# Kernel optimization log

Measured on AMD Instinct MI355X. Metric: run time of the kernel, lower is better.

The kernel has to match this reference:

```python
import jax, jax.numpy as jnp
import numpy as np

N_NODES = 100000
N_EDGES = 1600000
IN_CH = 128
HID = 128
OUT_CH = 10


def setup_inputs() -> dict:
    key = jax.random.key(0)
    ks = jax.random.split(key, 14)
    s_in = 1.0 / np.sqrt(IN_CH)
    s_h = 1.0 / np.sqrt(HID)
    return {
        "x0": jax.random.normal(ks[0], (N_NODES, IN_CH), jnp.float32),
        "edge_index": jax.random.randint(ks[1], (2, N_EDGES), 0, N_NODES, jnp.int32),
        "edge_weight": jax.random.uniform(ks[2], (N_EDGES,), jnp.float32),
        # GraphConv layer 1 (in -> hid): lin_rel (weight+bias) applied to aggregated msgs, lin_root (no bias)
        "W1_rel": jax.random.uniform(ks[3], (IN_CH, HID), jnp.float32, -s_in, s_in),
        "b1": jax.random.uniform(ks[4], (HID,), jnp.float32, -s_in, s_in),
        "W1_root": jax.random.uniform(ks[5], (IN_CH, HID), jnp.float32, -s_in, s_in),
        # GraphConv layer 2 (hid -> hid)
        "W2_rel": jax.random.uniform(ks[6], (HID, HID), jnp.float32, -s_h, s_h),
        "b2": jax.random.uniform(ks[7], (HID,), jnp.float32, -s_h, s_h),
        "W2_root": jax.random.uniform(ks[8], (HID, HID), jnp.float32, -s_h, s_h),
        # GraphConv layer 3 (hid -> hid)
        "W3_rel": jax.random.uniform(ks[9], (HID, HID), jnp.float32, -s_h, s_h),
        "b3": jax.random.uniform(ks[10], (HID,), jnp.float32, -s_h, s_h),
        "W3_root": jax.random.uniform(ks[11], (HID, HID), jnp.float32, -s_h, s_h),
        # classification head
        "W_lin": jax.random.uniform(ks[12], (HID, OUT_CH), jnp.float32, -s_h, s_h),
        "b_lin": jax.random.uniform(ks[13], (OUT_CH,), jnp.float32, -s_h, s_h),
    }


def _graph_conv(x, src, dst, ew, W_rel, b_rel, W_root):
    # message: x_j * w_e ; aggregate: scatter-add onto dst ; update: lin_rel(agg) + lin_root(x)
    msg = x[src] * ew[:, None]                                   # [E, C]
    agg = jax.ops.segment_sum(msg, dst, num_segments=x.shape[0])  # [N, C]
    return agg @ W_rel + b_rel + x @ W_root                      # [N, C']


def reference(x0, edge_index, edge_weight,
              W1_rel, b1, W1_root,
              W2_rel, b2, W2_root,
              W3_rel, b3, W3_root,
              W_lin, b_lin):
    src, dst = edge_index[0], edge_index[1]
    # dropout p=0.2 is identity in eval mode
    x1 = jax.nn.relu(_graph_conv(x0, src, dst, edge_weight, W1_rel, b1, W1_root))
    x2 = jax.nn.relu(_graph_conv(x1, src, dst, edge_weight, W2_rel, b2, W2_root))
    x3 = jax.nn.relu(_graph_conv(x2, src, dst, edge_weight, W3_rel, b3, W3_root))
    logits = x3 @ W_lin + b_lin
    return jax.nn.log_softmax(logits, axis=-1)
```

## Files before the change

### kernel.cpp

```cpp
#include <hip/hip_runtime.h>
#include <hip/hip_bf16.h>
#include <math.h>

#define C128 128
#define OUT_CH 10

typedef __attribute__((ext_vector_type(8))) short short8;
typedef __attribute__((ext_vector_type(4))) float f32x4;
typedef __attribute__((ext_vector_type(2))) float f32x2;
typedef __attribute__((ext_vector_type(4))) int i32x4;

__device__ __forceinline__ unsigned short f2bf(float f) {
    unsigned b = __float_as_uint(f);
    unsigned r = (b + 0x7FFF + ((b >> 16) & 1)) >> 16;
    return (unsigned short)r;
}
__device__ __forceinline__ float bf2f(unsigned short u) {
    return __uint_as_float(((unsigned)u) << 16);
}


#define NBMAX 400
#define BCAP  4608
#define P1K   4096

__global__ __launch_bounds__(512) void bin_kernel(
    const int* __restrict__ ei, const float* __restrict__ ew,
    int* __restrict__ gcur, uint2* __restrict__ bins, int E, int nb)
{
    __shared__ int cnt[NBMAX];
    __shared__ int pos[NBMAX];
    __shared__ int gbase[NBMAX];
    __shared__ int s[512];
    __shared__ int totalSh;
    __shared__ uint2 buf[P1K];

    const int t = threadIdx.x;
    const int e0 = blockIdx.x * P1K;

    for (int b = t; b < nb; b += 512) { cnt[b] = 0; pos[b] = 0; }
    __syncthreads();

    unsigned rec[8];
    int dstv[8];
    const int e = e0 + t * 8;
    if (e + 8 <= E) {
        i32x4 d0 = __builtin_nontemporal_load((const i32x4*)(ei + E + e));
        i32x4 d1 = __builtin_nontemporal_load((const i32x4*)(ei + E + e + 4));
        i32x4 s0 = __builtin_nontemporal_load((const i32x4*)(ei + e));
        i32x4 s1 = __builtin_nontemporal_load((const i32x4*)(ei + e + 4));
        f32x4 w0 = __builtin_nontemporal_load((const f32x4*)(ew + e));
        f32x4 w1 = __builtin_nontemporal_load((const f32x4*)(ew + e + 4));
        int dd[8] = {d0.x, d0.y, d0.z, d0.w, d1.x, d1.y, d1.z, d1.w};
        int ss[8] = {s0.x, s0.y, s0.z, s0.w, s1.x, s1.y, s1.z, s1.w};
        float ww[8] = {w0.x, w0.y, w0.z, w0.w, w1.x, w1.y, w1.z, w1.w};
#pragma unroll
        for (int j = 0; j < 8; ++j) {
            unsigned wb = __float_as_uint(ww[j]);
            unsigned r  = ((wb + 0x7FFF + ((wb >> 16) & 1)) >> 16) & 0x7FFFu;
            rec[j]  = (unsigned)ss[j] | (r << 17);
            dstv[j] = dd[j];
            atomicAdd(&cnt[dd[j] >> 8], 1);
        }
    } else {
#pragma unroll
        for (int j = 0; j < 8; ++j) {
            int ee = e + j;
            if (ee < E) {
                int dst = ei[E + ee];
                unsigned wb = __float_as_uint(ew[ee]);
                unsigned r  = ((wb + 0x7FFF + ((wb >> 16) & 1)) >> 16) & 0x7FFFu;
                rec[j]  = (unsigned)ei[ee] | (r << 17);
                dstv[j] = dst;
                atomicAdd(&cnt[dst >> 8], 1);
            } else {
                dstv[j] = -1;
            }
        }
    }
    __syncthreads();

    int c = (t < nb) ? cnt[t] : 0;
    s[t] = c;
    __syncthreads();
    for (int o = 1; o < 512; o <<= 1) {
        int u = (t >= o) ? s[t - o] : 0;
        __syncthreads();
        s[t] += u;
        __syncthreads();
    }
    if (t == nb - 1) totalSh = s[t];
    __syncthreads();

#pragma unroll
    for (int j = 0; j < 8; ++j) {
        if (dstv[j] >= 0) {
            int b = dstv[j] >> 8;
            int r = atomicAdd(&pos[b], 1);
            buf[s[b] - cnt[b] + r] = make_uint2(rec[j], (unsigned)dstv[j]);
        }
    }
    __syncthreads();

    if (t < nb) {
        int b = t + (int)((blockIdx.x * 131u) % (unsigned)nb);
        if (b >= nb) b -= nb;
        int cb = cnt[b];
        if (cb > 0) gbase[b] = atomicAdd(&gcur[b], cb);
    }
    __syncthreads();

    const int total = totalSh;
    for (int i = t; i < total; i += 512) {
        uint2 v = buf[i];
        int b = (int)(v.y >> 8);
        int dest = gbase[b] + (i - (s[b] - cnt[b]));
        if (dest < BCAP) bins[(size_t)b * BCAP + dest] = v;
    }
}

__global__ __launch_bounds__(512) void bucket_scan_kernel(
    const int* __restrict__ gcur, int* __restrict__ bbase,
    int* __restrict__ row_ptr, int nb, int N, int E)
{
    __shared__ int s[512];
    int t = threadIdx.x;
    int v = (t < nb) ? gcur[t] : 0;
    s[t] = v;
    __syncthreads();
    for (int o = 1; o < 512; o <<= 1) {
        int u = (t >= o) ? s[t - o] : 0;
        __syncthreads();
        s[t] += u;
        __syncthreads();
    }
    if (t < nb) bbase[t] = s[t] - v;
    if (t == 0) row_ptr[N] = E;
}

__global__ __launch_bounds__(256) void build_kernel(
    const uint2* __restrict__ bins, const int* __restrict__ gcur,
    const int* __restrict__ bbase, int* __restrict__ row_ptr,
    unsigned* __restrict__ csr, int N)
{
    __shared__ int rowCnt[256];
    __shared__ int rowOff[256];
    __shared__ int sc[256];
    __shared__ unsigned out[BCAP];

    const int b = blockIdx.x, t = threadIdx.x;
    int cnt = gcur[b];
    if (cnt > BCAP) cnt = BCAP;
    const int base = bbase[b];
    const uint2* mb = bins + (size_t)b * BCAP;

    rowCnt[t] = 0;
    __syncthreads();
    for (int i = t; i < cnt; i += 256) atomicAdd(&rowCnt[(int)(mb[i].y & 255u)], 1);
    __syncthreads();

    int v = rowCnt[t];
    sc[t] = v;
    __syncthreads();
    for (int o = 1; o < 256; o <<= 1) {
        int u = (t >= o) ? sc[t - o] : 0;
        __syncthreads();
        sc[t] += u;
        __syncthreads();
    }
    rowOff[t] = sc[t] - v;
    int idx = b * 256 + t;
    if (idx <= N) row_ptr[idx] = base + sc[t] - v;
    rowCnt[t] = 0;
    __syncthreads();

    for (int i = t; i < cnt; i += 256) {
        uint2 r = mb[i];
        int d = (int)(r.y & 255u);
        int k = atomicAdd(&rowCnt[d], 1);
        out[rowOff[d] + k] = r.x;
    }
    __syncthreads();

    for (int i = t; i < cnt; i += 256) csr[base + i] = out[i];
}


__global__ __launch_bounds__(256) void cvt_both_kernel(const float4* __restrict__ x,
                                                       ushort4* __restrict__ xb,
                                                       unsigned* __restrict__ xf8, int n4) {
    int i = blockIdx.x * blockDim.x + threadIdx.x;
    if (i < n4) {
        float4 v = x[i];
        ushort4 o;
        o.x = f2bf(v.x); o.y = f2bf(v.y); o.z = f2bf(v.z); o.w = f2bf(v.w);
        xb[i] = o;
        unsigned p = __builtin_amdgcn_cvt_pk_fp8_f32(v.x, v.y, 0, false);
        p = __builtin_amdgcn_cvt_pk_fp8_f32(v.z, v.w, p, true);
        xf8[i] = p;
    }
}


__global__ __launch_bounds__(256) void pack_w_kernel(const float* __restrict__ Wr,
                                                     const float* __restrict__ Wt,
                                                     unsigned short* __restrict__ Wp) {
    int idx = blockIdx.x * 256 + threadIdx.x;
    int j    = idx & 7;
    int n    = (idx >> 3) & 127;
    int quad = (idx >> 10) & 3;
    int ks   = idx >> 12;
    const float* W = (ks < 4) ? Wr : Wt;
    int k = (ks & 3) * 32 + quad * 8 + j;
    Wp[idx] = f2bf(W[(size_t)k * C128 + n]);
}


__global__ __launch_bounds__(256) void gather_fp8_kernel(
    const unsigned* __restrict__ xf8,
    const int* __restrict__ row_ptr,
    const unsigned* __restrict__ csr, unsigned short* __restrict__ aggb, int N)
{
    int node = blockIdx.x * 4 + (threadIdx.x >> 6);
    if (node >= N) return;
    int lane = threadIdx.x & 63;
    int g   = lane >> 4;
    int l16 = lane & 15;
    int i0  = row_ptr[node];
    int deg = row_ptr[node + 1] - i0;

    f32x2 acc2[4];
#pragma unroll
    for (int j = 0; j < 4; ++j) acc2[j] = (f32x2){0.f, 0.f};

    for (int base = 0; base < deg; base += 64) {
        int rem = deg - base; if (rem > 64) rem = 64;
        int rec = 0;
        if (base + lane < deg) rec = (int)csr[i0 + base + lane];

        int c = 0;
        for (; c + 16 <= rem; c += 16) {
            int s0 = __shfl(rec, c + g,      64);
            int s1 = __shfl(rec, c + 4 + g,  64);
            int s2 = __shfl(rec, c + 8 + g,  64);
            int s3 = __shfl(rec, c + 12 + g, 64);
            float w0 = __uint_as_float(((unsigned)s0 >> 17) << 16);
            float w1 = __uint_as_float(((unsigned)s1 >> 17) << 16);
            float w2 = __uint_as_float(((unsigned)s2 >> 17) << 16);
            float w3 = __uint_as_float(((unsigned)s3 >> 17) << 16);
            uint2 q0 = *(const uint2*)&xf8[(size_t)(s0 & 0x1FFFF) * 32 + l16 * 2];
            uint2 q1 = *(const uint2*)&xf8[(size_t)(s1 & 0x1FFFF) * 32 + l16 * 2];
            uint2 q2 = *(const uint2*)&xf8[(size_t)(s2 & 0x1FFFF) * 32 + l16 * 2];
            uint2 q3 = *(const uint2*)&xf8[(size_t)(s3 & 0x1FFFF) * 32 + l16 * 2];
#define ACCUM(q, wv)                                                         \
            {                                                                \
                f32x2 w2v = {(wv), (wv)};                                    \
                acc2[0] += __builtin_amdgcn_cvt_pk_f32_fp8((q).x, false) * w2v; \
                acc2[1] += __builtin_amdgcn_cvt_pk_f32_fp8((q).x, true)  * w2v; \
                acc2[2] += __builtin_amdgcn_cvt_pk_f32_fp8((q).y, false) * w2v; \
                acc2[3] += __builtin_amdgcn_cvt_pk_f32_fp8((q).y, true)  * w2v; \
            }
            ACCUM(q0, w0) ACCUM(q1, w1) ACCUM(q2, w2) ACCUM(q3, w3)
        }
        for (; c < rem; c += 4) {
            int idx = c + g;
            int im = idx & 63;
            int s = __shfl(rec, im, 64);
            float wv = __uint_as_float(((unsigned)s >> 17) << 16);
            if (idx >= rem) wv = 0.f;
            uint2 q = *(const uint2*)&xf8[(size_t)(s & 0x1FFFF) * 32 + l16 * 2];
            ACCUM(q, wv)
        }
#undef ACCUM
    }

#pragma unroll
    for (int j = 0; j < 4; ++j) {
        acc2[j].x += __shfl_xor(acc2[j].x, 16, 64);
        acc2[j].y += __shfl_xor(acc2[j].y, 16, 64);
        acc2[j].x += __shfl_xor(acc2[j].x, 32, 64);
        acc2[j].y += __shfl_xor(acc2[j].y, 32, 64);
    }
    if (g == 0) {
        uint4 o;
        o.x = (unsigned)f2bf(acc2[0].x) | ((unsigned)f2bf(acc2[0].y) << 16);
        o.y = (unsigned)f2bf(acc2[1].x) | ((unsigned)f2bf(acc2[1].y) << 16);
        o.z = (unsigned)f2bf(acc2[2].x) | ((unsigned)f2bf(acc2[2].y) << 16);
        o.w = (unsigned)f2bf(acc2[3].x) | ((unsigned)f2bf(acc2[3].y) << 16);
        *(uint4*)&aggb[(size_t)node * C128 + l16 * 8] = o;
    }
}


__global__ __launch_bounds__(256) void gemm_slim(
    const unsigned short* __restrict__ aggb, const unsigned short* __restrict__ xb,
    const unsigned short* __restrict__ Wp, const float* __restrict__ bias,
    unsigned short* __restrict__ outb, unsigned char* __restrict__ outf8, int N)
{
    const int t = threadIdx.x;
    const int w    = t >> 6;
    const int lane = t & 63;
    const int l15  = lane & 15;
    const int quad = lane >> 4;
    const int wnode0 = blockIdx.x * 64 + w * 16;

    int arow = wnode0 + l15;
    if (arow >= N) arow = N - 1;

    short8 a[8];
#pragma unroll
    for (int k = 0; k < 4; ++k)
        a[k] = *(const short8*)&aggb[(size_t)arow * C128 + k * 32 + quad * 8];
#pragma unroll
    for (int k = 0; k < 4; ++k)
        a[4 + k] = *(const short8*)&xb[(size_t)arow * C128 + k * 32 + quad * 8];

    float bv[8];
#pragma unroll
    for (int nt = 0; nt < 8; ++nt) bv[nt] = bias[nt * 16 + l15];

    f32x4 acc[8];
#pragma unroll
    for (int nt = 0; nt < 8; ++nt) acc[nt] = (f32x4){0.f, 0.f, 0.f, 0.f};

#pragma unroll
    for (int ks = 0; ks < 8; ++ks) {
#pragma unroll
        for (int nt = 0; nt < 8; ++nt) {
            short8 b = *(const short8*)&Wp[(((ks * 4 + quad) * 128) + nt * 16 + l15) * 8];
            acc[nt] = __builtin_amdgcn_mfma_f32_16x16x32_bf16(a[ks], b, acc[nt], 0, 0, 0);
        }
    }

#pragma unroll
    for (int r = 0; r < 4; ++r) {
        int row = wnode0 + quad * 4 + r;
        if (row < N) {
#pragma unroll
            for (int nt = 0; nt < 8; ++nt) {
                float v = fmaxf(acc[nt][r] + bv[nt], 0.f);
                outb[(size_t)row * C128 + nt * 16 + l15] = f2bf(v);
                if (outf8) {
                    unsigned p8 = __builtin_amdgcn_cvt_pk_fp8_f32(v, 0.f, 0, false);
                    outf8[(size_t)row * C128 + nt * 16 + l15] = (unsigned char)(p8 & 0xff);
                }
            }
        }
    }
}


__global__ __launch_bounds__(256) void head_kernel(
    const unsigned short* __restrict__ x, const float* __restrict__ Wl,
    const float* __restrict__ bl, float* __restrict__ out, int N)
{
    int n = blockIdx.x * blockDim.x + threadIdx.x;
    if (n >= N) return;
    float acc[OUT_CH];
#pragma unroll
    for (int c = 0; c < OUT_CH; ++c) acc[c] = bl[c];
    const ushort4* row = (const ushort4*)(x + (size_t)n * C128);
#pragma unroll 4
    for (int kk = 0; kk < 32; ++kk) {
        ushort4 u = row[kk];
        float vx = bf2f(u.x), vy = bf2f(u.y), vz = bf2f(u.z), vw = bf2f(u.w);
        int k = kk * 4;
#pragma unroll
        for (int c = 0; c < OUT_CH; ++c) {
            acc[c] += vx * Wl[(k + 0) * OUT_CH + c]
                    + vy * Wl[(k + 1) * OUT_CH + c]
                    + vz * Wl[(k + 2) * OUT_CH + c]
                    + vw * Wl[(k + 3) * OUT_CH + c];
        }
    }
    float m = acc[0];
#pragma unroll
    for (int c = 1; c < OUT_CH; ++c) m = fmaxf(m, acc[c]);
    float s = 0.f;
#pragma unroll
    for (int c = 0; c < OUT_CH; ++c) s += __expf(acc[c] - m);
    float lse = m + __logf(s);
#pragma unroll
    for (int c = 0; c < OUT_CH; ++c) out[(size_t)n * OUT_CH + c] = acc[c] - lse;
}


extern "C" void kernel_launch(void* const* d_in, const int* in_sizes, int n_in,
                              void* d_out, int out_size, void* d_ws, size_t ws_size,
                              hipStream_t stream) {
    const float* x0   = (const float*)d_in[0];
    const int*   ei   = (const int*)  d_in[1];
    const float* ew   = (const float*)d_in[2];
    const float* W1r  = (const float*)d_in[3];
    const float* b1   = (const float*)d_in[4];
    const float* W1t  = (const float*)d_in[5];
    const float* W2r  = (const float*)d_in[6];
    const float* b2   = (const float*)d_in[7];
    const float* W2t  = (const float*)d_in[8];
    const float* W3r  = (const float*)d_in[9];
    const float* b3   = (const float*)d_in[10];
    const float* W3t  = (const float*)d_in[11];
    const float* Wlin = (const float*)d_in[12];
    const float* blin = (const float*)d_in[13];

    const int N = in_sizes[0] / C128;
    const int E = in_sizes[1] / 2;
    const int nb = (N + 255) >> 8;

    char* ws = (char*)d_ws;
    size_t off = 0;
    auto alloc = [&](size_t bytes) {
        void* p = ws + off;
        off = (off + bytes + 255) & ~(size_t)255;
        return p;
    };
    size_t bb = (size_t)N * C128 * sizeof(unsigned short);
    size_t fb = (size_t)N * C128;
    unsigned short* aggb = (unsigned short*)alloc(bb);
    unsigned short* xb0  = (unsigned short*)alloc(bb);
    unsigned short* xb1  = (unsigned short*)alloc(bb);
    unsigned char*  xf8  = (unsigned char*)alloc(fb);
    unsigned short* Wp1  = (unsigned short*)alloc(32768 * 2);
    unsigned short* Wp2  = (unsigned short*)alloc(32768 * 2);
    unsigned short* Wp3  = (unsigned short*)alloc(32768 * 2);
    unsigned* csr  = (unsigned*)alloc((size_t)E * 4);
    int* row_ptr   = (int*)alloc((size_t)(N + 2) * 4);
    uint2* bins    = (uint2*)alloc((size_t)nb * BCAP * 8);
    int* gcur      = (int*)alloc((size_t)nb * 4);
    int* bbase     = (int*)alloc((size_t)nb * 4);

    hipMemsetAsync(gcur, 0, (size_t)nb * sizeof(int), stream);
    bin_kernel<<<(E + P1K - 1) / P1K, 512, 0, stream>>>(ei, ew, gcur, bins, E, nb);
    bucket_scan_kernel<<<1, 512, 0, stream>>>(gcur, bbase, row_ptr, nb, N, E);
    build_kernel<<<nb, 256, 0, stream>>>(bins, gcur, bbase, row_ptr, csr, N);

    cvt_both_kernel<<<(N * C128 / 4 + 255) / 256, 256, 0, stream>>>(
        (const float4*)x0, (ushort4*)xb0, (unsigned*)xf8, N * C128 / 4);
    pack_w_kernel<<<128, 256, 0, stream>>>(W1r, W1t, Wp1);
    pack_w_kernel<<<128, 256, 0, stream>>>(W2r, W2t, Wp2);
    pack_w_kernel<<<128, 256, 0, stream>>>(W3r, W3t, Wp3);

    int gatherGrid = (N + 3) / 4;
    int gemmGrid   = (N + 63) / 64;

    gather_fp8_kernel<<<gatherGrid, 256, 0, stream>>>(
        (const unsigned*)xf8, row_ptr, csr, aggb, N);
    gemm_slim<<<gemmGrid, 256, 0, stream>>>(aggb, xb0, Wp1, b1, xb1, xf8, N);
    gather_fp8_kernel<<<gatherGrid, 256, 0, stream>>>(
        (const unsigned*)xf8, row_ptr, csr, aggb, N);
    gemm_slim<<<gemmGrid, 256, 0, stream>>>(aggb, xb1, Wp2, b2, xb0, xf8, N);
    gather_fp8_kernel<<<gatherGrid, 256, 0, stream>>>(
        (const unsigned*)xf8, row_ptr, csr, aggb, N);
    gemm_slim<<<gemmGrid, 256, 0, stream>>>(aggb, xb0, Wp3, b3, xb1, nullptr, N);
    head_kernel<<<(N + 255) / 256, 256, 0, stream>>>(xb1, Wlin, blin, (float*)d_out, N);
}
```

Before: 388.1 us.

## Fuse final GEMM with classification head and split bin records into SoA

The last GraphConv GEMM now computes the ReLU output in registers and applies the 128x10 head plus log-softmax directly, using cross-lane shuffles to reduce partial dot products. This removes the write and re-read of the layer-3 bf16 activations and one kernel launch. Separately, the edge bin buffer is split from 8-byte records into a 4-byte record array plus a 1-byte destination array, cutting bin traffic. The fused epilogue adds shuffle reductions and redundant head-weight loads per lane.

```diff
diff --git a/kernel.cpp b/kernel.cpp
--- a/kernel.cpp
+++ b/kernel.cpp
@@ -26,7 +26,8 @@
 
 __global__ __launch_bounds__(512) void bin_kernel(
     const int* __restrict__ ei, const float* __restrict__ ew,
-    int* __restrict__ gcur, uint2* __restrict__ bins, int E, int nb)
+    int* __restrict__ gcur, unsigned* __restrict__ bins_rec,
+    unsigned char* __restrict__ bins_dst, int E, int nb)
 {
     __shared__ int cnt[NBMAX];
     __shared__ int pos[NBMAX];
@@ -115,7 +116,10 @@
         uint2 v = buf[i];
         int b = (int)(v.y >> 8);
         int dest = gbase[b] + (i - (s[b] - cnt[b]));
-        if (dest < BCAP) bins[(size_t)b * BCAP + dest] = v;
+        if (dest < BCAP) {
+            bins_rec[(size_t)b * BCAP + dest] = v.x;
+            bins_dst[(size_t)b * BCAP + dest] = (unsigned char)(v.y & 255u);
+        }
     }
 }
 
@@ -139,9 +143,9 @@
 }
 
 __global__ __launch_bounds__(256) void build_kernel(
-    const uint2* __restrict__ bins, const int* __restrict__ gcur,
-    const int* __restrict__ bbase, int* __restrict__ row_ptr,
-    unsigned* __restrict__ csr, int N)
+    const unsigned* __restrict__ bins_rec, const unsigned char* __restrict__ bins_dst,
+    const int* __restrict__ gcur, const int* __restrict__ bbase,
+    int* __restrict__ row_ptr, unsigned* __restrict__ csr, int N)
 {
     __shared__ int rowCnt[256];
     __shared__ int rowOff[256];
@@ -152,11 +156,12 @@
     int cnt = gcur[b];
     if (cnt > BCAP) cnt = BCAP;
     const int base = bbase[b];
-    const uint2* mb = bins + (size_t)b * BCAP;
+    const unsigned* mbr = bins_rec + (size_t)b * BCAP;
+    const unsigned char* mbd = bins_dst + (size_t)b * BCAP;
 
     rowCnt[t] = 0;
     __syncthreads();
-    for (int i = t; i < cnt; i += 256) atomicAdd(&rowCnt[(int)(mb[i].y & 255u)], 1);
+    for (int i = t; i < cnt; i += 256) atomicAdd(&rowCnt[(int)mbd[i]], 1);
     __syncthreads();
 
     int v = rowCnt[t];
@@ -175,10 +180,9 @@
     __syncthreads();
 
     for (int i = t; i < cnt; i += 256) {
-        uint2 r = mb[i];
-        int d = (int)(r.y & 255u);
+        int d = (int)mbd[i];
         int k = atomicAdd(&rowCnt[d], 1);
-        out[rowOff[d] + k] = r.x;
+        out[rowOff[d] + k] = mbr[i];
     }
     __syncthreads();
 
@@ -340,48 +344,92 @@
             for (int nt = 0; nt < 8; ++nt) {
                 float v = fmaxf(acc[nt][r] + bv[nt], 0.f);
                 outb[(size_t)row * C128 + nt * 16 + l15] = f2bf(v);
-                if (outf8) {
-                    unsigned p8 = __builtin_amdgcn_cvt_pk_fp8_f32(v, 0.f, 0, false);
-                    outf8[(size_t)row * C128 + nt * 16 + l15] = (unsigned char)(p8 & 0xff);
-                }
+                unsigned p8 = __builtin_amdgcn_cvt_pk_fp8_f32(v, 0.f, 0, false);
+                outf8[(size_t)row * C128 + nt * 16 + l15] = (unsigned char)(p8 & 0xff);
             }
         }
     }
 }
 
 
-__global__ __launch_bounds__(256) void head_kernel(
-    const unsigned short* __restrict__ x, const float* __restrict__ Wl,
-    const float* __restrict__ bl, float* __restrict__ out, int N)
+__global__ __launch_bounds__(256) void gemm_head(
+    const unsigned short* __restrict__ aggb, const unsigned short* __restrict__ xb,
+    const unsigned short* __restrict__ Wp, const float* __restrict__ bias,
+    const float* __restrict__ Wl, const float* __restrict__ bl,
+    float* __restrict__ out, int N)
 {
-    int n = blockIdx.x * blockDim.x + threadIdx.x;
-    if (n >= N) return;
-    float acc[OUT_CH];
-#pragma unroll
-    for (int c = 0; c < OUT_CH; ++c) acc[c] = bl[c];
-    const ushort4* row = (const ushort4*)(x + (size_t)n * C128);
-#pragma unroll 4
-    for (int kk = 0; kk < 32; ++kk) {
-        ushort4 u = row[kk];
-        float vx = bf2f(u.x), vy = bf2f(u.y), vz = bf2f(u.z), vw = bf2f(u.w);
-        int k = kk * 4;
+    const int t = threadIdx.x;
+    const int w    = t >> 6;
+    const int lane = t & 63;
+    const int l15  = lane & 15;
+    const int quad = lane >> 4;
+    const int wnode0 = blockIdx.x * 64 + w * 16;
+
+    int arow = wnode0 + l15;
+    if (arow >= N) arow = N - 1;
+
+    short8 a[8];
+#pragma unroll
+    for (int k = 0; k < 4; ++k)
+        a[k] = *(const short8*)&aggb[(size_t)arow * C128 + k * 32 + quad * 8];
+#pragma unroll
+    for (int k = 0; k < 4; ++k)
+        a[4 + k] = *(const short8*)&xb[(size_t)arow * C128 + k * 32 + quad * 8];
+
+    float bv[8];
+#pragma unroll
+    for (int nt = 0; nt < 8; ++nt) bv[nt] = bias[nt * 16 + l15];
+
+    f32x4 acc[8];
+#pragma unroll
+    for (int nt = 0; nt < 8; ++nt) acc[nt] = (f32x4){0.f, 0.f, 0.f, 0.f};
+
+#pragma unroll
+    for (int ks = 0; ks < 8; ++ks) {
+#pragma unroll
+        for (int nt = 0; nt < 8; ++nt) {
+            short8 b = *(const short8*)&Wp[(((ks * 4 + quad) * 128) + nt * 16 + l15) * 8];
+            acc[nt] = __builtin_amdgcn_mfma_f32_16x16x32_bf16(a[ks], b, acc[nt], 0, 0, 0);
+        }
+    }
+
+#pragma unroll
+    for (int r = 0; r < 4; ++r) {
+        int row = wnode0 + quad * 4 + r;
+        float part[OUT_CH];
+#pragma unroll
+        for (int c = 0; c < OUT_CH; ++c) part[c] = 0.f;
+#pragma unroll
+        for (int nt = 0; nt < 8; ++nt) {
+            float v = fmaxf(acc[nt][r] + bv[nt], 0.f);
+            const float* wrow = &Wl[(size_t)(nt * 16 + l15) * OUT_CH];
+#pragma unroll
+            for (int c = 0; c < OUT_CH; ++c) part[c] += v * wrow[c];
+        }
 #pragma unroll
         for (int c = 0; c < OUT_CH; ++c) {
-            acc[c] += vx * Wl[(k + 0) * OUT_CH + c]
-                    + vy * Wl[(k + 1) * OUT_CH + c]
-                    + vz * Wl[(k + 2) * OUT_CH + c]
-                    + vw * Wl[(k + 3) * OUT_CH + c];
-        }
-    }
-    float m = acc[0];
-#pragma unroll
-    for (int c = 1; c < OUT_CH; ++c) m = fmaxf(m, acc[c]);
-    float s = 0.f;
-#pragma unroll
-    for (int c = 0; c < OUT_CH; ++c) s += __expf(acc[c] - m);
-    float lse = m + __logf(s);
-#pragma unroll
-    for (int c = 0; c < OUT_CH; ++c) out[(size_t)n * OUT_CH + c] = acc[c] - lse;
+            part[c] += __shfl_xor(part[c], 1, 64);
+            part[c] += __shfl_xor(part[c], 2, 64);
+            part[c] += __shfl_xor(part[c], 4, 64);
+            part[c] += __shfl_xor(part[c], 8, 64);
+        }
+        if (l15 == 0 && row < N) {
+            float logits[OUT_CH];
+            float m = -1e30f;
+#pragma unroll
+            for (int c = 0; c < OUT_CH; ++c) {
+                logits[c] = part[c] + bl[c];
+                m = fmaxf(m, logits[c]);
+            }
+            float s = 0.f;
+#pragma unroll
+            for (int c = 0; c < OUT_CH; ++c) s += __expf(logits[c] - m);
+            float lse = m + __logf(s);
+#pragma unroll
+            for (int c = 0; c < OUT_CH; ++c)
+                out[(size_t)row * OUT_CH + c] = logits[c] - lse;
+        }
+    }
 }
 
 
@@ -425,14 +473,15 @@
     unsigned short* Wp3  = (unsigned short*)alloc(32768 * 2);
     unsigned* csr  = (unsigned*)alloc((size_t)E * 4);
     int* row_ptr   = (int*)alloc((size_t)(N + 2) * 4);
-    uint2* bins    = (uint2*)alloc((size_t)nb * BCAP * 8);
+    unsigned* bins_rec  = (unsigned*)alloc((size_t)nb * BCAP * 4);
+    unsigned char* bins_dst = (unsigned char*)alloc((size_t)nb * BCAP);
     int* gcur      = (int*)alloc((size_t)nb * 4);
     int* bbase     = (int*)alloc((size_t)nb * 4);
 
     hipMemsetAsync(gcur, 0, (size_t)nb * sizeof(int), stream);
-    bin_kernel<<<(E + P1K - 1) / P1K, 512, 0, stream>>>(ei, ew, gcur, bins, E, nb);
+    bin_kernel<<<(E + P1K - 1) / P1K, 512, 0, stream>>>(ei, ew, gcur, bins_rec, bins_dst, E, nb);
     bucket_scan_kernel<<<1, 512, 0, stream>>>(gcur, bbase, row_ptr, nb, N, E);
-    build_kernel<<<nb, 256, 0, stream>>>(bins, gcur, bbase, row_ptr, csr, N);
+    build_kernel<<<nb, 256, 0, stream>>>(bins_rec, bins_dst, gcur, bbase, row_ptr, csr, N);
 
     cvt_both_kernel<<<(N * C128 / 4 + 255) / 256, 256, 0, stream>>>(
         (const float4*)x0, (ushort4*)xb0, (unsigned*)xf8, N * C128 / 4);
@@ -451,6 +500,6 @@
     gemm_slim<<<gemmGrid, 256, 0, stream>>>(aggb, xb1, Wp2, b2, xb0, xf8, N);
     gather_fp8_kernel<<<gatherGrid, 256, 0, stream>>>(
         (const unsigned*)xf8, row_ptr, csr, aggb, N);
-    gemm_slim<<<gemmGrid, 256, 0, stream>>>(aggb, xb0, Wp3, b3, xb1, nullptr, N);
-    head_kernel<<<(N + 255) / 256, 256, 0, stream>>>(xb1, Wlin, blin, (float*)d_out, N);
-}
+    gemm_head<<<gemmGrid, 256, 0, stream>>>(aggb, xb0, Wp3, b3, Wlin, blin,
+                                            (float*)d_out, N);
+}
```

Measured after the change: 406.2 us. 4.7% more time.
